# Performance work log

Measured on AMD Instinct MI355X. Metric: run time of the kernel, lower is better.

Reference implementation:

```python
import jax, jax.numpy as jnp
import numpy as np

DIM = 256      # dim_hidden * 2
HEADS = 8      # hier_tf_head
C = 256        # out_channels per head (concat=False)
FF = 1024      # dim_hidden * 8
N_HOPS = 4096
HOP_LEN = 12
N_MEM = N_HOPS * HOP_LEN
N = N_HOPS + N_MEM  # 53248 total nodes


def setup_inputs() -> dict:
    key = jax.random.key(0)
    ks = jax.random.split(key, 8)
    x = jax.random.normal(ks[0], (N, DIM), jnp.float32)
    # hop_attn structure built by the python loops: [j,j] self-edges for hop
    # tokens, then one edge (member_node -> hop_token) per member.
    hop_self = np.stack([np.arange(N_HOPS), np.arange(N_HOPS)])
    mem_src = np.arange(N_HOPS, N)
    mem_dst = np.arange(N_MEM) // HOP_LEN
    edge_index = jnp.asarray(
        np.concatenate([hop_self, np.stack([mem_src, mem_dst])], axis=1),
        jnp.int32)  # [2, E]

    def init(k, shp, fan):
        return jax.random.normal(k, shp, jnp.float32) / np.sqrt(fan).astype(np.float32)

    return {
        "x": x,
        "edge_index": edge_index,
        "gat_W": init(ks[1], (DIM, HEADS * C), DIM),
        "gat_att_src": init(ks[2], (HEADS, C), C),
        "gat_att_dst": init(ks[3], (HEADS, C), C),
        "gat_bias": jnp.zeros((C,), jnp.float32),
        "ffn_W1": init(ks[4], (DIM, FF), DIM),
        "ffn_b1": jnp.zeros((FF,), jnp.float32),
        "ffn_W2": init(ks[5], (FF, DIM), FF),
        "ffn_b2": jnp.zeros((DIM,), jnp.float32),
        "ln1_g": jnp.ones((DIM,), jnp.float32),
        "ln1_b": jnp.zeros((DIM,), jnp.float32),
        "ln2_g": jnp.ones((DIM,), jnp.float32),
        "ln2_b": jnp.zeros((DIM,), jnp.float32),
    }


def _layer_norm(x, g, b, eps=1e-5):
    mu = jnp.mean(x, axis=-1, keepdims=True)
    var = jnp.mean(jnp.square(x - mu), axis=-1, keepdims=True)
    return (x - mu) * jax.lax.rsqrt(var + eps) * g + b


def _gat_conv(x, src, dst, W, att_src, att_dst, bias):
    # PyG GATConv, concat=False (mean over heads), negative_slope=0.2
    h = (x @ W).reshape(N, HEADS, C)                       # [N,H,C]
    a_s = jnp.einsum('nhc,hc->nh', h, att_src)             # [N,H]
    a_d = jnp.einsum('nhc,hc->nh', h, att_dst)
    e = jax.nn.leaky_relu(a_s[src] + a_d[dst], 0.2)        # [E,H]
    m = jax.ops.segment_max(e, dst, num_segments=N)        # per-dst softmax
    e = jnp.exp(e - m[dst])
    denom = jax.ops.segment_sum(e, dst, num_segments=N)
    alpha = e / (denom[dst] + 1e-16)                       # [E,H]
    agg = jax.ops.segment_sum(h[src] * alpha[:, :, None], dst, num_segments=N)
    return agg.mean(axis=1) + bias                         # [N,DIM]


def reference(x, edge_index, gat_W, gat_att_src, gat_att_dst, gat_bias,
              ffn_W1, ffn_b1, ffn_W2, ffn_b2, ln1_g, ln1_b, ln2_g, ln2_b):
    # GATConv adds self-loops for every node by default
    loops = jnp.arange(N, dtype=edge_index.dtype)
    src = jnp.concatenate([edge_index[0], loops])
    dst = jnp.concatenate([edge_index[1], loops])
    # GAT + residual + LN (dropout is identity at eval)
    g_out = _gat_conv(x, src, dst, gat_W, gat_att_src, gat_att_dst, gat_bias)
    x1 = _layer_norm(g_out + x, ln1_g, ln1_b)
    # FFN + residual + LN
    ff = jax.nn.relu(x1 @ ffn_W1 + ffn_b1) @ ffn_W2 + ffn_b2
    return _layer_norm(ff + x1, ln2_g, ln2_b)
```

## Files before the change

### kernel.cpp

```cpp
#include <hip/hip_runtime.h>
#include <cstdint>
#include <cstddef>

#define N_TOT   53248
#define N_HOPS  4096
#define HOP_LEN 12
#define NHEAD   8
#define FFD     1024
#define GLD     384

typedef __bf16 bf16x8 __attribute__((ext_vector_type(8)));
typedef float f32x4 __attribute__((ext_vector_type(4)));

__device__ __forceinline__ unsigned short f2bf(float f) {
    unsigned int u = __float_as_uint(f);
    u += 0x7FFFu + ((u >> 16) & 1u);
    return (unsigned short)(u >> 16);
}
__device__ __forceinline__ float bf2f(unsigned short b) {
    return __uint_as_float((unsigned int)b << 16);
}
__device__ __forceinline__ void gload16(const void* g, void* l) {
    __builtin_amdgcn_global_load_lds(
        (const __attribute__((address_space(1))) void*)g,
        (__attribute__((address_space(3))) void*)l, 16, 0, 0);
}

__global__ __launch_bounds__(256) void prep_w(
    const float* __restrict__ W, const float* __restrict__ att_s,
    const float* __restrict__ att_d, unsigned short* __restrict__ BcT)
{
    int d = blockIdx.x, c = threadIdx.x;
    int wave = c >> 6;
    __shared__ float ps4[4], pd4[4];
    float wm = 0.f;
    for (int h = 0; h < NHEAD; ++h) {
        float w = W[d * 2048 + h * 256 + c];
        wm += w;
        float ps = w * att_s[h * 256 + c];
        float pd = w * att_d[h * 256 + c];
        for (int o = 32; o > 0; o >>= 1) {
            ps += __shfl_xor(ps, o);
            pd += __shfl_xor(pd, o);
        }
        if ((c & 63) == 0) { ps4[wave] = ps; pd4[wave] = pd; }
        __syncthreads();
        if (c == 0) BcT[(256 + h) * 256 + d] = f2bf(ps4[0] + ps4[1] + ps4[2] + ps4[3]);
        if (c == 1) BcT[(264 + h) * 256 + d] = f2bf(pd4[0] + pd4[1] + pd4[2] + pd4[3]);
        __syncthreads();
    }
    BcT[c * 256 + d] = f2bf(wm * 0.125f);
}

__global__ __launch_bounds__(256) void tconv(
    const float* __restrict__ in, unsigned short* __restrict__ out,
    int IS, int OS, int in_zoff, int out_zoff)
{
    __shared__ float t[32][33];
    in  += (size_t)blockIdx.z * in_zoff;
    out += (size_t)blockIdx.z * out_zoff;
    int tx = threadIdx.x, ty = threadIdx.y;
    int c0 = blockIdx.x * 32, r0 = blockIdx.y * 32;
    #pragma unroll
    for (int k = 0; k < 4; ++k)
        t[ty + 8 * k][tx] = in[(size_t)(r0 + ty + 8 * k) * IS + c0 + tx];
    __syncthreads();
    #pragma unroll
    for (int k = 0; k < 4; ++k)
        out[(size_t)(c0 + ty + 8 * k) * OS + r0 + tx] = f2bf(t[tx][ty + 8 * k]);
}

__global__ __launch_bounds__(256) void cvt_bf16(
    const float* __restrict__ in, unsigned short* __restrict__ out, int n4)
{
    int i = blockIdx.x * 256 + threadIdx.x;
    if (i >= n4) return;
    float4 v = ((const float4*)in)[i];
    ushort4 o;
    o.x = f2bf(v.x); o.y = f2bf(v.y); o.z = f2bf(v.z); o.w = f2bf(v.w);
    ((ushort4*)out)[i] = o;
}

__global__ __launch_bounds__(256) void hop_z(
    const unsigned short* __restrict__ xb, const unsigned short* __restrict__ gb,
    unsigned short* __restrict__ z)
{
    int j = blockIdx.x, tid = threadIdx.x;
    __shared__ float xr[13][256];
    __shared__ float sm[NHEAD][13];
    __shared__ float walpha[NHEAD][13];
    __shared__ float mxs[NHEAD], invs[NHEAD];

    for (int i = tid; i < 13 * 32; i += 256) {
        int r = i >> 5, c8 = (i & 31) * 8;
        int src = (r == 0) ? j : (N_HOPS + j * HOP_LEN + r - 1);
        uint4 u = *(const uint4*)&xb[(size_t)src * 256 + c8];
        float4 lo, hi;
        lo.x = bf2f((unsigned short)(u.x & 0xFFFF)); lo.y = bf2f((unsigned short)(u.x >> 16));
        lo.z = bf2f((unsigned short)(u.y & 0xFFFF)); lo.w = bf2f((unsigned short)(u.y >> 16));
        hi.x = bf2f((unsigned short)(u.z & 0xFFFF)); hi.y = bf2f((unsigned short)(u.z >> 16));
        hi.z = bf2f((unsigned short)(u.w & 0xFFFF)); hi.w = bf2f((unsigned short)(u.w >> 16));
        *(float4*)&xr[r][c8] = lo;
        *(float4*)&xr[r][c8 + 4] = hi;
    }
    if (tid < NHEAD * 13) {
        int h = tid / 13, k = tid % 13;
        int src = (k == 0) ? j : (N_HOPS + j * HOP_LEN + k - 1);
        float ad = bf2f(gb[(size_t)j * GLD + 264 + h]);
        float v = bf2f(gb[(size_t)src * GLD + 256 + h]) + ad;
        sm[h][k] = v > 0.f ? v : 0.2f * v;
    }
    __syncthreads();
    if (tid < NHEAD) {
        int h = tid;
        float mx = sm[h][0];
        for (int k = 1; k < 13; ++k) mx = fmaxf(mx, sm[h][k]);
        float sum = 2.f * expf(sm[h][0] - mx);
        for (int k = 1; k < 13; ++k) sum += expf(sm[h][k] - mx);
        mxs[h] = mx;
        invs[h] = 0.125f / (sum + 1e-16f);
    }
    __syncthreads();
    if (tid < NHEAD * 13) {
        int h = tid / 13, k = tid % 13;
        walpha[h][k] = (k == 0 ? 2.f : 1.f) * expf(sm[h][k] - mxs[h]) * invs[h];
    }
    __syncthreads();
    for (int h = 0; h < NHEAD; ++h) {
        float acc = 0.f;
        #pragma unroll
        for (int r = 0; r < 13; ++r) acc += walpha[h][r] * xr[r][tid];
        z[((size_t)j * NHEAD + h) * 256 + tid] = f2bf(acc);
    }
}

template <int RELU, int OUT_BF16, int SWZ>
__global__ __launch_bounds__(256) void gemm_bt(
    const unsigned short* __restrict__ A, const unsigned short* __restrict__ BT,
    const float* __restrict__ bias, void* __restrict__ Cout,
    int M, int Nc, int K, int ldc)
{
    __shared__ __align__(16) unsigned short As[2][128 * 32];
    __shared__ __align__(16) unsigned short Bs[2][128 * 32];
    const int tid = threadIdx.x;
    const int l = tid & 63;
    int bm, bn;
    if (SWZ) {
        int lid = blockIdx.x + gridDim.x * blockIdx.y;
        int per = (gridDim.x * gridDim.y) >> 3;
        int wg = (lid & 7) * per + (lid >> 3);
        bm = (wg / gridDim.x) * 128;
        bn = (wg % gridDim.x) * 128;
    } else {
        bm = blockIdx.y * 128; bn = blockIdx.x * 128;
    }
    const int wm = ((tid >> 6) >> 1) * 64, wn = ((tid >> 6) & 1) * 64;

    const int r0 = tid >> 2, ke0 = (tid & 3) * 8;
    const int r1 = (256 + tid) >> 2, ke1 = ((256 + tid) & 3) * 8;
    const unsigned short* ga0 = A + (size_t)(bm + r0) * K + ke0;
    const unsigned short* ga1 = A + (size_t)(bm + r1) * K + ke1;
    const unsigned short* gb0 = BT + (size_t)(bn + r0) * K + ke0;
    const unsigned short* gb1 = BT + (size_t)(bn + r1) * K + ke1;

    f32x4 acc[4][4];
    #pragma unroll
    for (int m = 0; m < 4; ++m)
        #pragma unroll
        for (int n = 0; n < 4; ++n)
            acc[m][n] = (f32x4){0.f, 0.f, 0.f, 0.f};

    const int lrow = l & 15, lk8 = (l >> 4) * 8;

    gload16(ga0, &As[0][(size_t)tid * 8]);
    gload16(ga1, &As[0][(size_t)(256 + tid) * 8]);
    gload16(gb0, &Bs[0][(size_t)tid * 8]);
    gload16(gb1, &Bs[0][(size_t)(256 + tid) * 8]);

    int cur = 0;
    for (int k0 = 0; k0 < K; k0 += 32) {
        const int nxt = cur ^ 1;
        if (k0 + 32 < K) {
            gload16(ga0 + k0 + 32, &As[nxt][(size_t)tid * 8]);
            gload16(ga1 + k0 + 32, &As[nxt][(size_t)(256 + tid) * 8]);
            gload16(gb0 + k0 + 32, &Bs[nxt][(size_t)tid * 8]);
            gload16(gb1 + k0 + 32, &Bs[nxt][(size_t)(256 + tid) * 8]);
            asm volatile("s_waitcnt vmcnt(4)" ::: "memory");
        } else {
            asm volatile("s_waitcnt vmcnt(0)" ::: "memory");
        }
        __builtin_amdgcn_s_barrier();
        bf16x8 af[4], bfr[4];
        #pragma unroll
        for (int m = 0; m < 4; ++m)
            af[m] = *(const bf16x8*)&As[cur][(wm + m * 16 + lrow) * 32 + lk8];
        #pragma unroll
        for (int n = 0; n < 4; ++n)
            bfr[n] = *(const bf16x8*)&Bs[cur][(wn + n * 16 + lrow) * 32 + lk8];
        #pragma unroll
        for (int m = 0; m < 4; ++m)
            #pragma unroll
            for (int n = 0; n < 4; ++n)
                acc[m][n] = __builtin_amdgcn_mfma_f32_16x16x32_bf16(
                    af[m], bfr[n], acc[m][n], 0, 0, 0);
        __builtin_amdgcn_s_barrier();
        cur = nxt;
    }

    const int orow = (l >> 4) * 4, ocol = l & 15;
    #pragma unroll
    for (int m = 0; m < 4; ++m) {
        int gr = bm + wm + m * 16 + orow;
        #pragma unroll
        for (int n = 0; n < 4; ++n) {
            int gc = bn + wn + n * 16 + ocol;
            float bv = bias[gc];
            #pragma unroll
            for (int r = 0; r < 4; ++r) {
                float v = acc[m][n][r] + bv;
                if (RELU) v = fmaxf(v, 0.f);
                if (OUT_BF16)
                    ((unsigned short*)Cout)[(size_t)(gr + r) * ldc + gc] = f2bf(v);
                else
                    ((float*)Cout)[(size_t)(gr + r) * ldc + gc] = v;
            }
        }
    }
}

__global__ __launch_bounds__(256) void gemm_bt_sk(
    const unsigned short* __restrict__ A, const unsigned short* __restrict__ BT,
    unsigned short* __restrict__ Cpart, int M, int Nc, int Ksl, int ldA)
{
    __shared__ __align__(16) unsigned short As[2][128 * 32];
    __shared__ __align__(16) unsigned short Bs[2][128 * 32];
    const int tid = threadIdx.x;
    const int l = tid & 63;
    const int bm = blockIdx.y * 128, bn = blockIdx.x * 128;
    const int koff = blockIdx.z * Ksl;
    const int wm = ((tid >> 6) >> 1) * 64, wn = ((tid >> 6) & 1) * 64;

    const int r0 = tid >> 2, ke0 = (tid & 3) * 8;
    const int r1 = (256 + tid) >> 2, ke1 = ((256 + tid) & 3) * 8;
    const unsigned short* ga0 = A + (size_t)(bm + r0) * ldA + koff + ke0;
    const unsigned short* ga1 = A + (size_t)(bm + r1) * ldA + koff + ke1;
    const unsigned short* gb0 = BT + (size_t)(bn + r0) * ldA + koff + ke0;
    const unsigned short* gb1 = BT + (size_t)(bn + r1) * ldA + koff + ke1;

    f32x4 acc[4][4];
    #pragma unroll
    for (int m = 0; m < 4; ++m)
        #pragma unroll
        for (int n = 0; n < 4; ++n)
            acc[m][n] = (f32x4){0.f, 0.f, 0.f, 0.f};

    const int lrow = l & 15, lk8 = (l >> 4) * 8;

    gload16(ga0, &As[0][(size_t)tid * 8]);
    gload16(ga1, &As[0][(size_t)(256 + tid) * 8]);
    gload16(gb0, &Bs[0][(size_t)tid * 8]);
    gload16(gb1, &Bs[0][(size_t)(256 + tid) * 8]);

    int cur = 0;
    for (int k0 = 0; k0 < Ksl; k0 += 32) {
        const int nxt = cur ^ 1;
        if (k0 + 32 < Ksl) {
            gload16(ga0 + k0 + 32, &As[nxt][(size_t)tid * 8]);
            gload16(ga1 + k0 + 32, &As[nxt][(size_t)(256 + tid) * 8]);
            gload16(gb0 + k0 + 32, &Bs[nxt][(size_t)tid * 8]);
            gload16(gb1 + k0 + 32, &Bs[nxt][(size_t)(256 + tid) * 8]);
            asm volatile("s_waitcnt vmcnt(4)" ::: "memory");
        } else {
            asm volatile("s_waitcnt vmcnt(0)" ::: "memory");
        }
        __builtin_amdgcn_s_barrier();
        bf16x8 af[4], bfr[4];
        #pragma unroll
        for (int m = 0; m < 4; ++m)
            af[m] = *(const bf16x8*)&As[cur][(wm + m * 16 + lrow) * 32 + lk8];
        #pragma unroll
        for (int n = 0; n < 4; ++n)
            bfr[n] = *(const bf16x8*)&Bs[cur][(wn + n * 16 + lrow) * 32 + lk8];
        #pragma unroll
        for (int m = 0; m < 4; ++m)
            #pragma unroll
            for (int n = 0; n < 4; ++n)
                acc[m][n] = __builtin_amdgcn_mfma_f32_16x16x32_bf16(
                    af[m], bfr[n], acc[m][n], 0, 0, 0);
        __builtin_amdgcn_s_barrier();
        cur = nxt;
    }

    unsigned short* Cp = Cpart + (size_t)blockIdx.z * M * Nc;
    const int orow = (l >> 4) * 4, ocol = l & 15;
    #pragma unroll
    for (int m = 0; m < 4; ++m) {
        int gr = bm + wm + m * 16 + orow;
        #pragma unroll
        for (int n = 0; n < 4; ++n) {
            int gc = bn + wn + n * 16 + ocol;
            #pragma unroll
            for (int r = 0; r < 4; ++r)
                Cp[(size_t)(gr + r) * Nc + gc] = f2bf(acc[m][n][r]);
        }
    }
}

__global__ __launch_bounds__(256) void red_hop(
    const unsigned short* __restrict__ P, const float* __restrict__ bias,
    unsigned short* __restrict__ gbuf)
{
    int i = blockIdx.x * 256 + threadIdx.x;
    int row = i >> 6, c4 = (i & 63) * 4;
    float4 s = { 0.f, 0.f, 0.f, 0.f };
    #pragma unroll
    for (int zz = 0; zz < 8; ++zz) {
        ushort4 u = *(const ushort4*)&P[(size_t)zz * N_HOPS * 256 + (size_t)row * 256 + c4];
        s.x += bf2f(u.x); s.y += bf2f(u.y); s.z += bf2f(u.z); s.w += bf2f(u.w);
    }
    float4 bv = *(const float4*)&bias[c4];
    ushort4 o;
    o.x = f2bf(s.x + bv.x); o.y = f2bf(s.y + bv.y);
    o.z = f2bf(s.z + bv.z); o.w = f2bf(s.w + bv.w);
    *(ushort4*)&gbuf[(size_t)row * GLD + c4] = o;
}

__global__ __launch_bounds__(256) void ln_add_bb(
    const unsigned short* __restrict__ a, const unsigned short* __restrict__ b,
    const float* __restrict__ g, const float* __restrict__ be,
    unsigned short* __restrict__ outp)
{
    int wave = threadIdx.x >> 6, lane = threadIdx.x & 63;
    int n = blockIdx.x * 4 + wave;
    ushort4 av = *(const ushort4*)&a[(size_t)n * GLD + lane * 4];
    ushort4 bv = ((const ushort4*)b)[(size_t)n * 64 + lane];
    float v[4];
    v[0] = bf2f(av.x) + bf2f(bv.x); v[1] = bf2f(av.y) + bf2f(bv.y);
    v[2] = bf2f(av.z) + bf2f(bv.z); v[3] = bf2f(av.w) + bf2f(bv.w);
    float s = v[0] + v[1] + v[2] + v[3];
    for (int o = 32; o > 0; o >>= 1) s += __shfl_xor(s, o);
    float mu = s * (1.f / 256.f);
    float q = 0.f;
    #pragma unroll
    for (int i = 0; i < 4; ++i) { float d = v[i] - mu; q += d * d; }
    for (int o = 32; o > 0; o >>= 1) q += __shfl_xor(q, o);
    float rstd = rsqrtf(q * (1.f / 256.f) + 1e-5f);
    int c = lane * 4;
    float4 gv = *(const float4*)&g[c];
    float4 bev = *(const float4*)&be[c];
    ushort4 o4;
    o4.x = f2bf((v[0] - mu) * rstd * gv.x + bev.x);
    o4.y = f2bf((v[1] - mu) * rstd * gv.y + bev.y);
    o4.z = f2bf((v[2] - mu) * rstd * gv.z + bev.z);
    o4.w = f2bf((v[3] - mu) * rstd * gv.w + bev.w);
    ((ushort4*)outp)[(size_t)n * 64 + lane] = o4;
}

__global__ __launch_bounds__(512) void ffn2_ln(
    const unsigned short* __restrict__ hid, const unsigned short* __restrict__ W2T,
    const float* __restrict__ b2, const unsigned short* __restrict__ x1b,
    const float* __restrict__ g2, const float* __restrict__ be2,
    float* __restrict__ out)
{
    __shared__ __align__(16) unsigned short As[2][64 * 32];
    __shared__ __align__(16) unsigned short Bs[2][256 * 32];
    __shared__ float lnS[64][4], lnQ[64][4], lnM[64], lnR[64];

    const int tid = threadIdx.x, l = tid & 63, wid = tid >> 6;
    const int wr = wid >> 2, wc = wid & 3;
    const int lrow = l & 15, lk8 = (l >> 4) * 8;
    const int lid = blockIdx.x;
    const int row0 = ((lid & 7) * 104 + (lid >> 3)) * 64;

    const unsigned short* ga  = hid + (size_t)(row0 + (tid >> 2)) * FFD + (tid & 3) * 8;
    const unsigned short* gb0 = W2T + (size_t)(tid >> 2) * FFD + (tid & 3) * 8;
    const unsigned short* gb1 = W2T + (size_t)((512 + tid) >> 2) * FFD + ((512 + tid) & 3) * 8;

    f32x4 acc[2][4];
    #pragma unroll
    for (int m = 0; m < 2; ++m)
        #pragma unroll
        for (int n = 0; n < 4; ++n)
            acc[m][n] = (f32x4){0.f, 0.f, 0.f, 0.f};

    if (tid < 256) gload16(ga, &As[0][(size_t)tid * 8]);
    gload16(gb0, &Bs[0][(size_t)tid * 8]);
    gload16(gb1, &Bs[0][(size_t)(512 + tid) * 8]);

    int cur = 0;
    for (int k0 = 0; k0 < FFD; k0 += 32) {
        const int nxt = cur ^ 1;
        if (k0 + 32 < FFD) {
            if (tid < 256) gload16(ga + k0 + 32, &As[nxt][(size_t)tid * 8]);
            gload16(gb0 + k0 + 32, &Bs[nxt][(size_t)tid * 8]);
            gload16(gb1 + k0 + 32, &Bs[nxt][(size_t)(512 + tid) * 8]);
            if (tid < 256) asm volatile("s_waitcnt vmcnt(3)" ::: "memory");
            else           asm volatile("s_waitcnt vmcnt(2)" ::: "memory");
        } else {
            asm volatile("s_waitcnt vmcnt(0)" ::: "memory");
        }
        __builtin_amdgcn_s_barrier();
        bf16x8 af[2], bfr[4];
        #pragma unroll
        for (int m = 0; m < 2; ++m)
            af[m] = *(const bf16x8*)&As[cur][(wr * 32 + m * 16 + lrow) * 32 + lk8];
        #pragma unroll
        for (int n = 0; n < 4; ++n)
            bfr[n] = *(const bf16x8*)&Bs[cur][(wc * 64 + n * 16 + lrow) * 32 + lk8];
        #pragma unroll
        for (int m = 0; m < 2; ++m)
            #pragma unroll
            for (int n = 0; n < 4; ++n)
                acc[m][n] = __builtin_amdgcn_mfma_f32_16x16x32_bf16(
                    af[m], bfr[n], acc[m][n], 0, 0, 0);
        __builtin_amdgcn_s_barrier();
        cur = nxt;
    }

    const int orow = (l >> 4) * 4, ocol = l & 15;
    float b2c[4], g2c[4], be2c[4];
    #pragma unroll
    for (int n = 0; n < 4; ++n) {
        int col = wc * 64 + n * 16 + ocol;
        b2c[n] = b2[col]; g2c[n] = g2[col]; be2c[n] = be2[col];
    }
    #pragma unroll
    for (int m = 0; m < 2; ++m)
        #pragma unroll
        for (int r = 0; r < 4; ++r) {
            int row = wr * 32 + m * 16 + orow + r;
            #pragma unroll
            for (int n = 0; n < 4; ++n) {
                int col = wc * 64 + n * 16 + ocol;
                float res = bf2f(x1b[(size_t)(row0 + row) * 256 + col]);
                acc[m][n][r] += b2c[n] + res;
            }
        }
    #pragma unroll
    for (int m = 0; m < 2; ++m)
        #pragma unroll
        for (int r = 0; r < 4; ++r) {
            float s = 0.f, q = 0.f;
            #pragma unroll
            for (int n = 0; n < 4; ++n) {
                float v = acc[m][n][r];
                s += v; q += v * v;
            }
            #pragma unroll
            for (int o = 8; o >= 1; o >>= 1) {
                s += __shfl_xor(s, o);
                q += __shfl_xor(q, o);
            }
            if (ocol == 0) {
                int row = wr * 32 + m * 16 + orow + r;
                lnS[row][wc] = s; lnQ[row][wc] = q;
            }
        }
    __syncthreads();
    if (tid < 64) {
        float s = lnS[tid][0] + lnS[tid][1] + lnS[tid][2] + lnS[tid][3];
        float q = lnQ[tid][0] + lnQ[tid][1] + lnQ[tid][2] + lnQ[tid][3];
        float mu = s * (1.f / 256.f);
        lnM[tid] = mu;
        lnR[tid] = rsqrtf(q * (1.f / 256.f) - mu * mu + 1e-5f);
    }
    __syncthreads();
    #pragma unroll
    for (int m = 0; m < 2; ++m)
        #pragma unroll
        for (int r = 0; r < 4; ++r) {
            int row = wr * 32 + m * 16 + orow + r;
            float mu = lnM[row], rs = lnR[row];
            #pragma unroll
            for (int n = 0; n < 4; ++n) {
                int col = wc * 64 + n * 16 + ocol;
                out[(size_t)(row0 + row) * 256 + col] =
                    (acc[m][n][r] - mu) * rs * g2c[n] + be2c[n];
            }
        }
}

extern "C" void kernel_launch(void* const* d_in, const int* in_sizes, int n_in,
                              void* d_out, int out_size, void* d_ws, size_t ws_size,
                              hipStream_t stream)
{
    const float* x       = (const float*)d_in[0];
    const float* gat_W   = (const float*)d_in[2];
    const float* att_src = (const float*)d_in[3];
    const float* att_dst = (const float*)d_in[4];
    const float* gat_b   = (const float*)d_in[5];
    const float* W1      = (const float*)d_in[6];
    const float* b1      = (const float*)d_in[7];
    const float* W2      = (const float*)d_in[8];
    const float* b2      = (const float*)d_in[9];
    const float* ln1_g   = (const float*)d_in[10];
    const float* ln1_b   = (const float*)d_in[11];
    const float* ln2_g   = (const float*)d_in[12];
    const float* ln2_b   = (const float*)d_in[13];
    float* out = (float*)d_out;

    char* p = (char*)d_ws;
    auto carve = [&p](size_t bytes) { char* r = p; p += (bytes + 255) & ~(size_t)255; return r; };
    unsigned short* gbuf = (unsigned short*)carve((size_t)N_TOT * GLD * 2);
    unsigned short* x1b  = (unsigned short*)carve((size_t)N_TOT * 256 * 2);
    unsigned short* z    = (unsigned short*)carve((size_t)N_HOPS * 2048 * 2);
    unsigned short* hopP = (unsigned short*)carve((size_t)8 * N_HOPS * 256 * 2);
    unsigned short* hid  = (unsigned short*)carve((size_t)N_TOT * FFD * 2);
    unsigned short* BcT  = (unsigned short*)carve((size_t)GLD * 256 * 2);
    unsigned short* B2T  = (unsigned short*)carve((size_t)2048 * 256 * 2);
    unsigned short* W1T  = (unsigned short*)carve((size_t)FFD * 256 * 2);
    unsigned short* W2T  = (unsigned short*)carve((size_t)256 * FFD * 2);
    float*          bias384 = (float*)carve(GLD * 4);

    hipMemsetAsync(BcT + 272 * 256, 0, (size_t)(GLD - 272) * 256 * 2, stream);
    hipMemcpyAsync(bias384, gat_b, 256 * 4, hipMemcpyDeviceToDevice, stream);
    hipMemsetAsync(bias384 + 256, 0, (GLD - 256) * 4, stream);
    hipLaunchKernelGGL(prep_w, dim3(256), dim3(256), 0, stream,
                       gat_W, att_src, att_dst, BcT);
    hipLaunchKernelGGL(tconv, dim3(8, 8, 8), dim3(32, 8), 0, stream,
                       gat_W, B2T, 2048, 2048, 256, 256);
    hipLaunchKernelGGL(tconv, dim3(32, 8, 1), dim3(32, 8), 0, stream,
                       W1, W1T, 1024, 256, 0, 0);
    hipLaunchKernelGGL(tconv, dim3(8, 32, 1), dim3(32, 8), 0, stream,
                       W2, W2T, 256, 1024, 0, 0);
    hipLaunchKernelGGL(cvt_bf16, dim3(N_TOT * 256 / 4 / 256), dim3(256), 0, stream,
                       x, x1b, N_TOT * 256 / 4);
    hipLaunchKernelGGL((gemm_bt<0, 1, 1>), dim3(GLD / 128, N_TOT / 128), dim3(256), 0, stream,
                       x1b, BcT, bias384, gbuf, N_TOT, GLD, 256, GLD);
    hipLaunchKernelGGL(hop_z, dim3(N_HOPS), dim3(256), 0, stream,
                       x1b, gbuf, z);
    hipLaunchKernelGGL(gemm_bt_sk, dim3(2, N_HOPS / 128, 8), dim3(256), 0, stream,
                       z, B2T, hopP, N_HOPS, 256, 256, 2048);
    hipLaunchKernelGGL(red_hop, dim3(N_HOPS * 64 / 256), dim3(256), 0, stream,
                       hopP, gat_b, gbuf);
    hipLaunchKernelGGL(ln_add_bb, dim3(N_TOT / 4), dim3(256), 0, stream,
                       gbuf, x1b, ln1_g, ln1_b, x1b);
    hipLaunchKernelGGL((gemm_bt<1, 1, 1>), dim3(FFD / 128, N_TOT / 128), dim3(256), 0, stream,
                       x1b, W1T, b1, hid, N_TOT, FFD, 256, FFD);
    hipLaunchKernelGGL(ffn2_ln, dim3(N_TOT / 64), dim3(512), 0, stream,
                       hid, W2T, b2, x1b, ln2_g, ln2_b, out);
    (void)in_sizes; (void)n_in; (void)out_size; (void)ws_size;
}
```

Baseline: 223.2 us.

## Deepen ffn2_ln prefetch pipeline and XOR-swizzle LDS tiles

Result: no change. 224.8 us (+0.7%).

```diff
diff --git a/kernel.cpp b/kernel.cpp
--- a/kernel.cpp
+++ b/kernel.cpp
@@ -362,19 +362,22 @@
     const float* __restrict__ g2, const float* __restrict__ be2,
     float* __restrict__ out)
 {
-    __shared__ __align__(16) unsigned short As[2][64 * 32];
-    __shared__ __align__(16) unsigned short Bs[2][256 * 32];
+    __shared__ __align__(16) unsigned short As[6][64 * 32];
+    __shared__ __align__(16) unsigned short Bs[3][256 * 32];
     __shared__ float lnS[64][4], lnQ[64][4], lnM[64], lnR[64];
 
     const int tid = threadIdx.x, l = tid & 63, wid = tid >> 6;
     const int wr = wid >> 2, wc = wid & 3;
-    const int lrow = l & 15, lk8 = (l >> 4) * 8;
+    const int lrow = l & 15, hi16 = l >> 4;
     const int lid = blockIdx.x;
     const int row0 = ((lid & 7) * 104 + (lid >> 3)) * 64;
 
-    const unsigned short* ga  = hid + (size_t)(row0 + (tid >> 2)) * FFD + (tid & 3) * 8;
-    const unsigned short* gb0 = W2T + (size_t)(tid >> 2) * FFD + (tid & 3) * 8;
-    const unsigned short* gb1 = W2T + (size_t)((512 + tid) >> 2) * FFD + ((512 + tid) & 3) * 8;
+    const int agr = tid >> 2;
+    const int asl = (tid & 3) ^ (agr & 3);
+    const unsigned short* ga = hid + (size_t)(row0 + agr) * FFD + asl * 8;
+    const int bsl = (tid & 3) ^ ((tid >> 2) & 3);
+    const unsigned short* gb0 = W2T + (size_t)(tid >> 2) * FFD + bsl * 8;
+    const unsigned short* gb1 = W2T + (size_t)((512 + tid) >> 2) * FFD + bsl * 8;
 
     f32x4 acc[2][4];
     #pragma unroll
@@ -383,41 +386,55 @@
         for (int n = 0; n < 4; ++n)
             acc[m][n] = (f32x4){0.f, 0.f, 0.f, 0.f};
 
-    if (tid < 256) gload16(ga, &As[0][(size_t)tid * 8]);
+    if (tid < 256) {
+        gload16(ga +   0, &As[0][(size_t)tid * 8]);
+        gload16(ga +  32, &As[1][(size_t)tid * 8]);
+        gload16(ga +  64, &As[2][(size_t)tid * 8]);
+        gload16(ga +  96, &As[3][(size_t)tid * 8]);
+    }
     gload16(gb0, &Bs[0][(size_t)tid * 8]);
     gload16(gb1, &Bs[0][(size_t)(512 + tid) * 8]);
-
-    int cur = 0;
-    for (int k0 = 0; k0 < FFD; k0 += 32) {
-        const int nxt = cur ^ 1;
-        if (k0 + 32 < FFD) {
-            if (tid < 256) gload16(ga + k0 + 32, &As[nxt][(size_t)tid * 8]);
-            gload16(gb0 + k0 + 32, &Bs[nxt][(size_t)tid * 8]);
-            gload16(gb1 + k0 + 32, &Bs[nxt][(size_t)(512 + tid) * 8]);
-            if (tid < 256) asm volatile("s_waitcnt vmcnt(3)" ::: "memory");
-            else           asm volatile("s_waitcnt vmcnt(2)" ::: "memory");
-        } else {
-            asm volatile("s_waitcnt vmcnt(0)" ::: "memory");
-        }
+    if (tid < 256) gload16(ga + 128, &As[4][(size_t)tid * 8]);
+    gload16(gb0 + 32, &Bs[1][(size_t)tid * 8]);
+    gload16(gb1 + 32, &Bs[1][(size_t)(512 + tid) * 8]);
+
+    int aC = 0, bC = 0, aS = 5, bS = 2;
+    for (int t = 0; t < 32; ++t) {
+        const int ka = (t + 5 <= 31) ? (t + 5) : 31;
+        const int kb = (t + 2 <= 31) ? (t + 2) : 31;
+        if (tid < 256) gload16(ga + ka * 32, &As[aS][(size_t)tid * 8]);
+        gload16(gb0 + kb * 32, &Bs[bS][(size_t)tid * 8]);
+        gload16(gb1 + kb * 32, &Bs[bS][(size_t)(512 + tid) * 8]);
+        if (tid < 256) asm volatile("s_waitcnt vmcnt(6)" ::: "memory");
+        else           asm volatile("s_waitcnt vmcnt(4)" ::: "memory");
         __builtin_amdgcn_s_barrier();
         bf16x8 af[2], bfr[4];
         #pragma unroll
-        for (int m = 0; m < 2; ++m)
-            af[m] = *(const bf16x8*)&As[cur][(wr * 32 + m * 16 + lrow) * 32 + lk8];
-        #pragma unroll
-        for (int n = 0; n < 4; ++n)
-            bfr[n] = *(const bf16x8*)&Bs[cur][(wc * 64 + n * 16 + lrow) * 32 + lk8];
+        for (int m = 0; m < 2; ++m) {
+            int row = wr * 32 + m * 16 + lrow;
+            af[m] = *(const bf16x8*)&As[aC][row * 32 + ((hi16 ^ (row & 3)) * 8)];
+        }
+        #pragma unroll
+        for (int n = 0; n < 4; ++n) {
+            int fc = wc * 64 + n * 16 + lrow;
+            bfr[n] = *(const bf16x8*)&Bs[bC][fc * 32 + ((hi16 ^ (fc & 3)) * 8)];
+        }
+        __builtin_amdgcn_s_setprio(1);
         #pragma unroll
         for (int m = 0; m < 2; ++m)
             #pragma unroll
             for (int n = 0; n < 4; ++n)
                 acc[m][n] = __builtin_amdgcn_mfma_f32_16x16x32_bf16(
                     af[m], bfr[n], acc[m][n], 0, 0, 0);
+        __builtin_amdgcn_s_setprio(0);
         __builtin_amdgcn_s_barrier();
-        cur = nxt;
-    }
-
-    const int orow = (l >> 4) * 4, ocol = l & 15;
+        aC = (aC == 5) ? 0 : aC + 1;
+        aS = (aS == 5) ? 0 : aS + 1;
+        bC = (bC == 2) ? 0 : bC + 1;
+        bS = (bS == 2) ? 0 : bS + 1;
+    }
+
+    const int orow = hi16 * 4, ocol = l & 15;
     float b2c[4], g2c[4], be2c[4];
     #pragma unroll
     for (int n = 0; n < 4; ++n) {
```

## Use 256x256 macro-tiles with 8 waves for FFN GEMMs

Applied to the files above, without the earlier changes.

After: 261.4 us. +17.1%, slower.

```diff
diff --git a/kernel.cpp b/kernel.cpp
--- a/kernel.cpp
+++ b/kernel.cpp
@@ -356,94 +356,206 @@
     ((ushort4*)outp)[(size_t)n * 64 + lane] = o4;
 }
 
-__global__ __launch_bounds__(512) void ffn2_ln(
+__global__ __launch_bounds__(512, 1) void gemm256(
+    const unsigned short* __restrict__ A, const unsigned short* __restrict__ BT,
+    const float* __restrict__ bias, unsigned short* __restrict__ C,
+    int Nc, int K, int ldc)
+{
+    __shared__ __align__(16) unsigned short As[2][256 * 64];
+    __shared__ __align__(16) unsigned short Bs[2][256 * 64];
+
+    const int tid = threadIdx.x, l = tid & 63, w = tid >> 6;
+    const int wr = w >> 2, wc = w & 3;
+    const int lrow = l & 15, hi16 = l >> 4;
+
+    const int gx = gridDim.x;
+    const int lid = blockIdx.x + gx * blockIdx.y;
+    const int per = (gx * gridDim.y) >> 3;
+    const int wg = (lid & 7) * per + (lid >> 3);
+    const int bm = (wg / gx) * 256, bn = (wg % gx) * 256;
+
+    const unsigned short* sA[4];
+    const unsigned short* sB[4];
+    #pragma unroll
+    for (int i = 0; i < 4; ++i) {
+        int g = i * 512 + tid, row = g >> 3, slot = g & 7;
+        sA[i] = A + (size_t)(bm + row) * K + slot * 8;
+        sB[i] = BT + (size_t)(bn + row) * K + slot * 8;
+    }
+
+    f32x4 acc[8][4];
+    #pragma unroll
+    for (int m = 0; m < 8; ++m)
+        #pragma unroll
+        for (int n = 0; n < 4; ++n)
+            acc[m][n] = (f32x4){0.f, 0.f, 0.f, 0.f};
+
+    #pragma unroll
+    for (int i = 0; i < 4; ++i) {
+        int g = i * 512 + tid;
+        gload16(sA[i], &As[0][(size_t)g * 8]);
+        gload16(sB[i], &Bs[0][(size_t)g * 8]);
+    }
+    asm volatile("s_waitcnt vmcnt(0)" ::: "memory");
+    __builtin_amdgcn_s_barrier();
+
+    const int KT = K >> 6;
+    int cur = 0;
+    for (int kt = 0; kt < KT; ++kt) {
+        if (kt + 1 < KT) {
+            #pragma unroll
+            for (int i = 0; i < 4; ++i) {
+                int g = i * 512 + tid;
+                gload16(sA[i] + (kt + 1) * 64, &As[cur ^ 1][(size_t)g * 8]);
+                gload16(sB[i] + (kt + 1) * 64, &Bs[cur ^ 1][(size_t)g * 8]);
+            }
+        }
+        #pragma unroll
+        for (int kk = 0; kk < 2; ++kk) {
+            bf16x8 bfr[4];
+            #pragma unroll
+            for (int n = 0; n < 4; ++n) {
+                int col = wc * 64 + n * 16 + lrow;
+                bfr[n] = *(const bf16x8*)&Bs[cur][col * 64 + kk * 32 + hi16 * 8];
+            }
+            #pragma unroll
+            for (int mh = 0; mh < 2; ++mh) {
+                bf16x8 af[4];
+                #pragma unroll
+                for (int mi = 0; mi < 4; ++mi) {
+                    int row = wr * 128 + (mh * 4 + mi) * 16 + lrow;
+                    af[mi] = *(const bf16x8*)&As[cur][row * 64 + kk * 32 + hi16 * 8];
+                }
+                __builtin_amdgcn_s_setprio(1);
+                #pragma unroll
+                for (int mi = 0; mi < 4; ++mi)
+                    #pragma unroll
+                    for (int n = 0; n < 4; ++n)
+                        acc[mh * 4 + mi][n] = __builtin_amdgcn_mfma_f32_16x16x32_bf16(
+                            af[mi], bfr[n], acc[mh * 4 + mi][n], 0, 0, 0);
+                __builtin_amdgcn_s_setprio(0);
+            }
+        }
+        asm volatile("s_waitcnt vmcnt(0)" ::: "memory");
+        __builtin_amdgcn_s_barrier();
+        cur ^= 1;
+    }
+
+    #pragma unroll
+    for (int n = 0; n < 4; ++n) {
+        int col = bn + wc * 64 + n * 16 + lrow;
+        float bv = bias[col];
+        #pragma unroll
+        for (int m = 0; m < 8; ++m) {
+            #pragma unroll
+            for (int r = 0; r < 4; ++r) {
+                int row = bm + wr * 128 + m * 16 + hi16 * 4 + r;
+                float v = fmaxf(acc[m][n][r] + bv, 0.f);
+                C[(size_t)row * ldc + col] = f2bf(v);
+            }
+        }
+    }
+}
+
+__global__ __launch_bounds__(512, 1) void ffn2_ln256(
     const unsigned short* __restrict__ hid, const unsigned short* __restrict__ W2T,
     const float* __restrict__ b2, const unsigned short* __restrict__ x1b,
     const float* __restrict__ g2, const float* __restrict__ be2,
     float* __restrict__ out)
 {
-    __shared__ __align__(16) unsigned short As[2][64 * 32];
-    __shared__ __align__(16) unsigned short Bs[2][256 * 32];
-    __shared__ float lnS[64][4], lnQ[64][4], lnM[64], lnR[64];
-
-    const int tid = threadIdx.x, l = tid & 63, wid = tid >> 6;
-    const int wr = wid >> 2, wc = wid & 3;
-    const int lrow = l & 15, lk8 = (l >> 4) * 8;
-    const int lid = blockIdx.x;
-    const int row0 = ((lid & 7) * 104 + (lid >> 3)) * 64;
-
-    const unsigned short* ga  = hid + (size_t)(row0 + (tid >> 2)) * FFD + (tid & 3) * 8;
-    const unsigned short* gb0 = W2T + (size_t)(tid >> 2) * FFD + (tid & 3) * 8;
-    const unsigned short* gb1 = W2T + (size_t)((512 + tid) >> 2) * FFD + ((512 + tid) & 3) * 8;
-
-    f32x4 acc[2][4];
-    #pragma unroll
-    for (int m = 0; m < 2; ++m)
+    __shared__ __align__(16) unsigned short As[2][256 * 64];
+    __shared__ __align__(16) unsigned short Bs[2][256 * 64];
+    __shared__ float lnS[256][4], lnQ[256][4], lnM[256], lnR[256];
+
+    const int tid = threadIdx.x, l = tid & 63, w = tid >> 6;
+    const int wr = w >> 2, wc = w & 3;
+    const int lrow = l & 15, hi16 = l >> 4;
+    const int row0 = blockIdx.x * 256;
+
+    const unsigned short* sA[4];
+    const unsigned short* sB[4];
+    #pragma unroll
+    for (int i = 0; i < 4; ++i) {
+        int g = i * 512 + tid, row = g >> 3, slot = g & 7;
+        sA[i] = hid + (size_t)(row0 + row) * FFD + slot * 8;
+        sB[i] = W2T + (size_t)row * FFD + slot * 8;
+    }
+
+    f32x4 acc[8][4];
+    #pragma unroll
+    for (int m = 0; m < 8; ++m)
         #pragma unroll
         for (int n = 0; n < 4; ++n)
             acc[m][n] = (f32x4){0.f, 0.f, 0.f, 0.f};
 
-    if (tid < 256) gload16(ga, &As[0][(size_t)tid * 8]);
-    gload16(gb0, &Bs[0][(size_t)tid * 8]);
-    gload16(gb1, &Bs[0][(size_t)(512 + tid) * 8]);
+    #pragma unroll
+    for (int i = 0; i < 4; ++i) {
+        int g = i * 512 + tid;
+        gload16(sA[i], &As[0][(size_t)g * 8]);
+        gload16(sB[i], &Bs[0][(size_t)g * 8]);
+    }
+    asm volatile("s_waitcnt vmcnt(0)" ::: "memory");
+    __builtin_amdgcn_s_barrier();
 
     int cur = 0;
-    for (int k0 = 0; k0 < FFD; k0 += 32) {
-        const int nxt = cur ^ 1;
-        if (k0 + 32 < FFD) {
-            if (tid < 256) gload16(ga + k0 + 32, &As[nxt][(size_t)tid * 8]);
-            gload16(gb0 + k0 + 32, &Bs[nxt][(size_t)tid * 8]);
-            gload16(gb1 + k0 + 32, &Bs[nxt][(size_t)(512 + tid) * 8]);
-            if (tid < 256) asm volatile("s_waitcnt vmcnt(3)" ::: "memory");
-            else           asm volatile("s_waitcnt vmcnt(2)" ::: "memory");
-        } else {
-            asm volatile("s_waitcnt vmcnt(0)" ::: "memory");
-        }
+    for (int kt = 0; kt < 16; ++kt) {
+        if (kt + 1 < 16) {
+            #pragma unroll
+            for (int i = 0; i < 4; ++i) {
+                int g = i * 512 + tid;
+                gload16(sA[i] + (kt + 1) * 64, &As[cur ^ 1][(size_t)g * 8]);
+                gload16(sB[i] + (kt + 1) * 64, &Bs[cur ^ 1][(size_t)g * 8]);
+            }
+        }
+        #pragma unroll
+        for (int kk = 0; kk < 2; ++kk) {
+            bf16x8 bfr[4];
+            #pragma unroll
+            for (int n = 0; n < 4; ++n) {
+                int col = wc * 64 + n * 16 + lrow;
+                bfr[n] = *(const bf16x8*)&Bs[cur][col * 64 + kk * 32 + hi16 * 8];
+            }
+            #pragma unroll
+            for (int mh = 0; mh < 2; ++mh) {
+                bf16x8 af[4];
+                #pragma unroll
+                for (int mi = 0; mi < 4; ++mi) {
+                    int row = wr * 128 + (mh * 4 + mi) * 16 + lrow;
+                    af[mi] = *(const bf16x8*)&As[cur][row * 64 + kk * 32 + hi16 * 8];
+                }
+                __builtin_amdgcn_s_setprio(1);
+                #pragma unroll
+                for (int mi = 0; mi < 4; ++mi)
+                    #pragma unroll
+                    for (int n = 0; n < 4; ++n)
+                        acc[mh * 4 + mi][n] = __builtin_amdgcn_mfma_f32_16x16x32_bf16(
+                            af[mi], bfr[n], acc[mh * 4 + mi][n], 0, 0, 0);
+                __builtin_amdgcn_s_setprio(0);
+            }
+        }
+        asm volatile("s_waitcnt vmcnt(0)" ::: "memory");
         __builtin_amdgcn_s_barrier();
-        bf16x8 af[2], bfr[4];
-        #pragma unroll
-        for (int m = 0; m < 2; ++m)
-            af[m] = *(const bf16x8*)&As[cur][(wr * 32 + m * 16 + lrow) * 32 + lk8];
-        #pragma unroll
-        for (int n = 0; n < 4; ++n)
-            bfr[n] = *(const bf16x8*)&Bs[cur][(wc * 64 + n * 16 + lrow) * 32 + lk8];
-        #pragma unroll
-        for (int m = 0; m < 2; ++m)
-            #pragma unroll
-            for (int n = 0; n < 4; ++n)
-                acc[m][n] = __builtin_amdgcn_mfma_f32_16x16x32_bf16(
-                    af[m], bfr[n], acc[m][n], 0, 0, 0);
-        __builtin_amdgcn_s_barrier();
-        cur = nxt;
-    }
-
-    const int orow = (l >> 4) * 4, ocol = l & 15;
+        cur ^= 1;
+    }
+
     float b2c[4], g2c[4], be2c[4];
     #pragma unroll
     for (int n = 0; n < 4; ++n) {
-        int col = wc * 64 + n * 16 + ocol;
+        int col = wc * 64 + n * 16 + lrow;
         b2c[n] = b2[col]; g2c[n] = g2[col]; be2c[n] = be2[col];
     }
     #pragma unroll
-    for (int m = 0; m < 2; ++m)
+    for (int m = 0; m < 8; ++m) {
         #pragma unroll
         for (int r = 0; r < 4; ++r) {
-            int row = wr * 32 + m * 16 + orow + r;
+            int row = wr * 128 + m * 16 + hi16 * 4 + r;
+            float s = 0.f, q = 0.f;
             #pragma unroll
             for (int n = 0; n < 4; ++n) {
-                int col = wc * 64 + n * 16 + ocol;
-                float res = bf2f(x1b[(size_t)(row0 + row) * 256 + col]);
-                acc[m][n][r] += b2c[n] + res;
-            }
-        }
-    #pragma unroll
-    for (int m = 0; m < 2; ++m)
-        #pragma unroll
-        for (int r = 0; r < 4; ++r) {
-            float s = 0.f, q = 0.f;
-            #pragma unroll
-            for (int n = 0; n < 4; ++n) {
-                float v = acc[m][n][r];
+                int col = wc * 64 + n * 16 + lrow;
+                float v = acc[m][n][r] + b2c[n]
+                        + bf2f(x1b[(size_t)(row0 + row) * 256 + col]);
+                acc[m][n][r] = v;
                 s += v; q += v * v;
             }
             #pragma unroll
@@ -451,13 +563,13 @@
                 s += __shfl_xor(s, o);
                 q += __shfl_xor(q, o);
             }
-            if (ocol == 0) {
-                int row = wr * 32 + m * 16 + orow + r;
+            if (lrow == 0) {
                 lnS[row][wc] = s; lnQ[row][wc] = q;
             }
         }
+    }
     __syncthreads();
-    if (tid < 64) {
+    if (tid < 256) {
         float s = lnS[tid][0] + lnS[tid][1] + lnS[tid][2] + lnS[tid][3];
         float q = lnQ[tid][0] + lnQ[tid][1] + lnQ[tid][2] + lnQ[tid][3];
         float mu = s * (1.f / 256.f);
@@ -466,18 +578,19 @@
     }
     __syncthreads();
     #pragma unroll
-    for (int m = 0; m < 2; ++m)
+    for (int m = 0; m < 8; ++m) {
         #pragma unroll
         for (int r = 0; r < 4; ++r) {
-            int row = wr * 32 + m * 16 + orow + r;
+            int row = wr * 128 + m * 16 + hi16 * 4 + r;
             float mu = lnM[row], rs = lnR[row];
             #pragma unroll
             for (int n = 0; n < 4; ++n) {
-                int col = wc * 64 + n * 16 + ocol;
+                int col = wc * 64 + n * 16 + lrow;
                 out[(size_t)(row0 + row) * 256 + col] =
                     (acc[m][n][r] - mu) * rs * g2c[n] + be2c[n];
             }
         }
+    }
 }
 
 extern "C" void kernel_launch(void* const* d_in, const int* in_sizes, int n_in,
@@ -535,9 +648,9 @@
                        hopP, gat_b, gbuf);
     hipLaunchKernelGGL(ln_add_bb, dim3(N_TOT / 4), dim3(256), 0, stream,
                        gbuf, x1b, ln1_g, ln1_b, x1b);
-    hipLaunchKernelGGL((gemm_bt<1, 1, 1>), dim3(FFD / 128, N_TOT / 128), dim3(256), 0, stream,
-                       x1b, W1T, b1, hid, N_TOT, FFD, 256, FFD);
-    hipLaunchKernelGGL(ffn2_ln, dim3(N_TOT / 64), dim3(512), 0, stream,
+    hipLaunchKernelGGL(gemm256, dim3(FFD / 256, N_TOT / 256), dim3(512), 0, stream,
+                       x1b, W1T, b1, hid, FFD, 256, FFD);
+    hipLaunchKernelGGL(ffn2_ln256, dim3(N_TOT / 256), dim3(512), 0, stream,
                        hid, W2T, b2, x1b, ln2_g, ln2_b, out);
     (void)in_sizes; (void)n_in; (void)out_size; (void)ws_size;
 }
```
